# Optimization experiments

Measured on AMD Instinct MI355X. Metric: run time of the kernel, lower is better.

The kernel has to match this reference:

```python
import jax, jax.numpy as jnp
import numpy as np

K = 7            # kernel size per spatial dim
HALF = K // 2    # 3
WIN = K * K      # 49


def _rel_dist():
    # matches torch: meshgrid('ij') of arange(k)-k//2, euclidean dist, flattened row-major
    c = np.arange(K, dtype=np.float32) - HALF
    gi, gj = np.meshgrid(c, c, indexing='ij')
    return jnp.asarray(np.sqrt(gi ** 2 + gj ** 2).reshape(-1))


def _unfold2d(t):
    B, H, W, C = t.shape
    p = jnp.pad(t, ((0, 0), (HALF, HALF), (HALF, HALF), (0, 0)))
    wins = [p[:, i:i + H, j:j + W, :] for i in range(K) for j in range(K)]
    return jnp.stack(wins, axis=3)


def setup_inputs() -> dict:
    key = jax.random.key(0)
    k1, k2, k3, k4, k5 = jax.random.split(key, 5)
    B, H, W, C = 4, 64, 64, 128
    x = jax.random.normal(k1, (B, H, W, C), dtype=jnp.float32)
    W_qkv = jax.random.normal(k2, (C, 3 * C), dtype=jnp.float32) * (C ** -0.5)
    # width_proj is zero-initialized in the module; use small random values to exercise the soft mask
    W_width = jax.random.normal(k3, (C, 1), dtype=jnp.float32) * 0.02
    b_width = jax.random.normal(k4, (1,), dtype=jnp.float32) * 0.02
    W_out = jax.random.normal(k5, (C, C), dtype=jnp.float32) * (C ** -0.5)
    return {"x": x, "W_qkv": W_qkv, "W_width": W_width, "b_width": b_width, "W_out": W_out}


def reference(x, W_qkv, W_width, b_width, W_out):
    B, H, W, C = x.shape
    L = H * W
    scale = C ** -0.5
    rel_dist = _rel_dist()
    max_dist = rel_dist.max()

    qkv = x @ W_qkv                              # (B,H,W,3C)
    q, k, v = jnp.split(qkv, 3, axis=-1)
    width = jax.nn.sigmoid(x @ W_width + b_width) * max_dist + 0.5  # (B,H,W,1)

    k_win = _unfold2d(k).reshape(B, L, WIN, C)
    v_win = _unfold2d(v).reshape(B, L, WIN, C)
    q_flat = q.reshape(B, L, C)
    width_flat = width.reshape(B, L, 1)

    scores = jnp.einsum('blc,blwc->blw', q_flat, k_win) * scale
    soft_mask = jax.nn.sigmoid((width_flat - rel_dist) * 5.0)
    scores = scores - (1.0 - soft_mask) * 10000.0
    attn = jax.nn.softmax(scores, axis=-1)
    out = jnp.einsum('blw,blwc->blc', attn, v_win).reshape(B, H, W, C)
    return (out + v) @ W_out
```

## Files before the change

kernel.cpp:

```cpp
#include <hip/hip_runtime.h>

#define C 128
#define NPIX 16384
#define THREE_C 384

typedef unsigned short u16;
typedef unsigned int u32;
typedef short bf16x8 __attribute__((ext_vector_type(8)));
typedef float f32x4 __attribute__((ext_vector_type(4)));

__device__ __forceinline__ float bf2f(u16 h) { return __uint_as_float(((u32)h) << 16); }
__device__ __forceinline__ u16 f2bf(float f) {
    u32 b = __float_as_uint(f);
    b += 0x7FFF + ((b >> 16) & 1);
    return (u16)(b >> 16);
}
__device__ __forceinline__ u32 pack2(float a, float b) {
    return (u32)f2bf(a) | ((u32)f2bf(b) << 16);
}

#define GST 136

__global__ __launch_bounds__(512) void qkv_kernel(const float* __restrict__ x,
                                                  const float* __restrict__ Wqkv,
                                                  const float* __restrict__ Wwidth,
                                                  const float* __restrict__ bwidth,
                                                  u16* __restrict__ qb,
                                                  u16* __restrict__ kb,
                                                  u16* __restrict__ vb,
                                                  float* __restrict__ width_g) {
    __shared__ u16 xs[128 * GST];
    __shared__ u16 wt[128 * GST];
    const int task = ((int)(blockIdx.x & 7)) * 48 + ((int)blockIdx.x >> 3);
    const int rb = task / 3;
    const int nb = task % 3;
    const int p0 = rb * 128;
    const int tid = threadIdx.x;
    const int wv = tid >> 6;
    const int l = tid & 63;
    const int l15 = l & 15;
    const int l4 = l >> 4;

    for (int f = tid; f < 4096; f += 512) {
        const int kq = f & 31, r = f >> 5;
        const float4 xv = *(const float4*)(x + (size_t)(p0 + r) * C + kq * 4);
        uint2 pk;
        pk.x = pack2(xv.x, xv.y);
        pk.y = pack2(xv.z, xv.w);
        *(uint2*)&xs[r * GST + kq * 4] = pk;
    }
    for (int f = tid; f < 4096; f += 512) {
        const int c = f & 127, kq = f >> 7;
        const float w0 = Wqkv[(size_t)(kq * 4 + 0) * THREE_C + nb * 128 + c];
        const float w1 = Wqkv[(size_t)(kq * 4 + 1) * THREE_C + nb * 128 + c];
        const float w2 = Wqkv[(size_t)(kq * 4 + 2) * THREE_C + nb * 128 + c];
        const float w3 = Wqkv[(size_t)(kq * 4 + 3) * THREE_C + nb * 128 + c];
        uint2 pk;
        pk.x = pack2(w0, w1);
        pk.y = pack2(w2, w3);
        *(uint2*)&wt[c * GST + kq * 4] = pk;
    }
    __syncthreads();

    if (nb == 0 && tid < 128) {
        float wacc = 0.f;
#pragma unroll
        for (int kk = 0; kk < C; ++kk) wacc += bf2f(xs[tid * GST + kk]) * Wwidth[kk];
        const float z = wacc + bwidth[0];
        width_g[p0 + tid] = (1.f / (1.f + __expf(-z))) * 4.242640687f + 0.5f;
    }

    const int strip = wv * 16;
    bf16x8 af[4];
#pragma unroll
    for (int kf = 0; kf < 4; ++kf)
        af[kf] = *(const bf16x8*)&xs[(strip + l15) * GST + kf * 32 + l4 * 8];

    f32x4 acc[8];
#pragma unroll
    for (int nf = 0; nf < 8; ++nf) acc[nf] = (f32x4){0.f, 0.f, 0.f, 0.f};
#pragma unroll
    for (int nf = 0; nf < 8; ++nf) {
#pragma unroll
        for (int kf = 0; kf < 4; ++kf) {
            const bf16x8 bf = *(const bf16x8*)&wt[(nf * 16 + l15) * GST + kf * 32 + l4 * 8];
            acc[nf] = __builtin_amdgcn_mfma_f32_16x16x32_bf16(af[kf], bf, acc[nf], 0, 0, 0);
        }
    }

    u16* dst = (nb == 0) ? qb : (nb == 1) ? kb : vb;
#pragma unroll
    for (int nf = 0; nf < 8; ++nf) {
        const int col = nf * 16 + l15;
#pragma unroll
        for (int r = 0; r < 4; ++r) {
            const int row = strip + l4 * 4 + r;
            dst[(size_t)(p0 + row) * C + col] = f2bf(acc[nf][r]);
        }
    }
}

#define HSTRIDE 136
#define TSTRIDE 232
#define VSWZ(ch, h) ((h) ^ ((((ch) >> 3) & 3) << 3))

__global__ __launch_bounds__(1024) void attn_kernel(const u16* __restrict__ qb,
                                                    const u16* __restrict__ kb,
                                                    const u16* __restrict__ vb,
                                                    const float* __restrict__ width_g,
                                                    const float* __restrict__ Wout,
                                                    float* __restrict__ out) {
    __shared__ u16 Kl[208 * HSTRIDE];
    __shared__ u16 Vt[128 * TSTRIDE];
    __shared__ u16 Pl[64 * TSTRIDE];
    __shared__ float rmax[4][64];
    __shared__ float rsum[4][64];
    __shared__ float wdl[64];

    const int tid = threadIdx.x;
    const int wv = tid >> 6;
    const int l = tid & 63;
    const int l15 = l & 15;
    const int l4 = l >> 4;

    const int W = ((int)blockIdx.x & 7) * 32 + ((int)blockIdx.x >> 3);
    const int b = W >> 6;
    const int t = W & 63;
    const int i0 = (t >> 3) * 8;
    const int j0 = (t & 7) * 8;
    const int pbase = b * 4096;

    if (tid < 64)
        wdl[tid] = width_g[pbase + (i0 + (tid >> 3)) * 64 + j0 + (tid & 7)];

    for (int f = tid; f < 3328; f += 1024) {
        const int c = f & 15, h = f >> 4;
        uint4 val = make_uint4(0, 0, 0, 0);
        if (h < 196) {
            const int hi = (h * 2341) >> 15;
            const int hj = h - hi * 14;
            const int ii = i0 - 3 + hi, jj = j0 - 3 + hj;
            if (((unsigned)ii < 64u) && ((unsigned)jj < 64u))
                val = *(const uint4*)(kb + (size_t)(pbase + ii * 64 + jj) * C + c * 8);
        }
        *(uint4*)&Kl[h * HSTRIDE + c * 8] = val;
    }
    for (int f = tid; f < 1792; f += 1024) {
        const int c8 = f & 15, h2 = f >> 4;
        const int h = h2 * 2;
        union { uint4 u4; u16 us[8]; } va, vz;
        va.u4 = make_uint4(0, 0, 0, 0);
        vz.u4 = make_uint4(0, 0, 0, 0);
        if (h < 196) {
            const int hi = (h * 2341) >> 15;
            const int hj = h - hi * 14;
            const int ii = i0 - 3 + hi, jj = j0 - 3 + hj;
            if (((unsigned)ii < 64u) && ((unsigned)jj < 64u))
                va.u4 = *(const uint4*)(vb + (size_t)(pbase + ii * 64 + jj) * C + c8 * 8);
        }
        if (h + 1 < 196) {
            const int hi = ((h + 1) * 2341) >> 15;
            const int hj = h + 1 - hi * 14;
            const int ii = i0 - 3 + hi, jj = j0 - 3 + hj;
            if (((unsigned)ii < 64u) && ((unsigned)jj < 64u))
                vz.u4 = *(const uint4*)(vb + (size_t)(pbase + ii * 64 + jj) * C + c8 * 8);
        }
#pragma unroll
        for (int s = 0; s < 8; ++s) {
            const int ch = c8 * 8 + s;
            *(u32*)&Vt[ch * TSTRIDE + VSWZ(ch, h)] = (u32)va.us[s] | ((u32)vz.us[s] << 16);
        }
    }

    const int strip = wv >> 2;
    const int g = wv & 3;
    bf16x8 qf[4];
    {
        const int qr = strip * 16 + l15;
        const int p = pbase + (i0 + (qr >> 3)) * 64 + j0 + (qr & 7);
#pragma unroll
        for (int kf = 0; kf < 4; ++kf)
            qf[kf] = *(const bf16x8*)(qb + (size_t)p * C + kf * 32 + l4 * 8);
    }
    __syncthreads();

    f32x4 sv[4];
#pragma unroll
    for (int tt = 0; tt < 4; ++tt) {
        const int nf = g + 4 * tt;
        f32x4 acc = {0.f, 0.f, 0.f, 0.f};
        if (nf < 13) {
            const u16* kr = Kl + (nf * 16 + l15) * HSTRIDE + l4 * 8;
#pragma unroll
            for (int kf = 0; kf < 4; ++kf)
                acc = __builtin_amdgcn_mfma_f32_16x16x32_bf16(
                    qf[kf], *(const bf16x8*)(kr + kf * 32), acc, 0, 0, 0);
        }
        sv[tt] = acc;
    }

    const int qrb = strip * 16 + l4 * 4;
    float wdr[4], mxr[4];
#pragma unroll
    for (int r = 0; r < 4; ++r) { wdr[r] = wdl[qrb + r]; mxr[r] = -3.0e38f; }
#pragma unroll
    for (int tt = 0; tt < 4; ++tt) {
        const int nf = g + 4 * tt;
        if (nf < 13) {
            const int n = nf * 16 + l15;
            const int hi = (n * 2341) >> 15;
            const int hj = n - hi * 14;
#pragma unroll
            for (int r = 0; r < 4; ++r) {
                const int qr = qrb + r;
                const int di = hi - 3 - (qr >> 3);
                const int dj = hj - 3 - (qr & 7);
                const bool valid = ((unsigned)(di + 3) <= 6u) && ((unsigned)(dj + 3) <= 6u);
                float s = -3.0e38f;
                if (valid) {
                    const float rd = sqrtf((float)(di * di + dj * dj));
                    const float sm = 1.f / (1.f + __expf(-5.f * (wdr[r] - rd)));
                    s = sv[tt][r] * 0.08838834765f - (1.f - sm) * 10000.f;
                }
                sv[tt][r] = s;
                mxr[r] = fmaxf(mxr[r], s);
            }
        } else {
#pragma unroll
            for (int r = 0; r < 4; ++r) sv[tt][r] = -3.0e38f;
        }
    }
#pragma unroll
    for (int r = 0; r < 4; ++r) {
        float m = mxr[r];
        m = fmaxf(m, __shfl_xor(m, 1));
        m = fmaxf(m, __shfl_xor(m, 2));
        m = fmaxf(m, __shfl_xor(m, 4));
        m = fmaxf(m, __shfl_xor(m, 8));
        mxr[r] = m;
    }
    float smr[4] = {0.f, 0.f, 0.f, 0.f};
#pragma unroll
    for (int tt = 0; tt < 4; ++tt) {
#pragma unroll
        for (int r = 0; r < 4; ++r) {
            const float e = __expf(sv[tt][r] - mxr[r]);
            sv[tt][r] = e;
            smr[r] += e;
        }
    }
#pragma unroll
    for (int r = 0; r < 4; ++r) {
        float s = smr[r];
        s += __shfl_xor(s, 1);
        s += __shfl_xor(s, 2);
        s += __shfl_xor(s, 4);
        s += __shfl_xor(s, 8);
        smr[r] = s;
    }
    if (l15 == 0) {
#pragma unroll
        for (int r = 0; r < 4; ++r) {
            rmax[g][qrb + r] = mxr[r];
            rsum[g][qrb + r] = smr[r];
        }
    }
    __syncthreads();

    u16* wtl = Kl;
    for (int f = tid; f < 4096; f += 1024) {
        const int c = f & 127, kq = f >> 7;
        const float w0 = Wout[(size_t)(kq * 4 + 0) * C + c];
        const float w1 = Wout[(size_t)(kq * 4 + 1) * C + c];
        const float w2 = Wout[(size_t)(kq * 4 + 2) * C + c];
        const float w3 = Wout[(size_t)(kq * 4 + 3) * C + c];
        uint2 pk;
        pk.x = pack2(w0, w1);
        pk.y = pack2(w2, w3);
        *(uint2*)&wtl[c * GST + kq * 4] = pk;
    }

    float fac[4];
#pragma unroll
    for (int r = 0; r < 4; ++r) {
        const int qr = qrb + r;
        const float m0 = rmax[0][qr], m1 = rmax[1][qr], m2 = rmax[2][qr], m3 = rmax[3][qr];
        const float mf = fmaxf(fmaxf(m0, m1), fmaxf(m2, m3));
        const float tot = rsum[0][qr] * __expf(m0 - mf) + rsum[1][qr] * __expf(m1 - mf)
                        + rsum[2][qr] * __expf(m2 - mf) + rsum[3][qr] * __expf(m3 - mf);
        fac[r] = __expf(mxr[r] - mf) / tot;
    }
#pragma unroll
    for (int tt = 0; tt < 4; ++tt) {
        const int nf = g + 4 * tt;
        if (nf < 13) {
            const int n = nf * 16 + l15;
#pragma unroll
            for (int r = 0; r < 4; ++r)
                Pl[(qrb + r) * TSTRIDE + n] = f2bf(sv[tt][r] * fac[r]);
        } else if (nf == 13) {
            const int n = 208 + l15;
#pragma unroll
            for (int r = 0; r < 4; ++r)
                Pl[(qrb + r) * TSTRIDE + n] = 0;
        }
    }
    __syncthreads();

    f32x4 oacc[2];
    oacc[0] = (f32x4){0.f, 0.f, 0.f, 0.f};
    oacc[1] = (f32x4){0.f, 0.f, 0.f, 0.f};
#pragma unroll
    for (int kf = 0; kf < 7; ++kf) {
        const bf16x8 pa = *(const bf16x8*)(Pl + (strip * 16 + l15) * TSTRIDE + kf * 32 + l4 * 8);
#pragma unroll
        for (int nf2 = 0; nf2 < 2; ++nf2) {
            const int ch = g * 32 + nf2 * 16 + l15;
            const bf16x8 vf = *(const bf16x8*)(Vt + ch * TSTRIDE + VSWZ(ch, kf * 32 + l4 * 8));
            oacc[nf2] = __builtin_amdgcn_mfma_f32_16x16x32_bf16(pa, vf, oacc[nf2], 0, 0, 0);
        }
    }

    u16* ylds = Kl + 128 * GST;
#pragma unroll
    for (int nf2 = 0; nf2 < 2; ++nf2) {
        const int cch = g * 32 + nf2 * 16 + l15;
#pragma unroll
        for (int r = 0; r < 4; ++r) {
            const int qr = qrb + r;
            const int h = 45 + (qr >> 3) * 14 + (qr & 7);
            const float vv = bf2f(Vt[cch * TSTRIDE + VSWZ(cch, h)]);
            ylds[qr * GST + cch] = f2bf(oacc[nf2][r] + vv);
        }
    }
    __syncthreads();

    bf16x8 yf[4];
#pragma unroll
    for (int kf = 0; kf < 4; ++kf)
        yf[kf] = *(const bf16x8*)&ylds[(strip * 16 + l15) * GST + kf * 32 + l4 * 8];

    f32x4 oc[2];
    oc[0] = (f32x4){0.f, 0.f, 0.f, 0.f};
    oc[1] = (f32x4){0.f, 0.f, 0.f, 0.f};
#pragma unroll
    for (int u = 0; u < 2; ++u) {
        const int nf = g + 4 * u;
#pragma unroll
        for (int kf = 0; kf < 4; ++kf) {
            const bf16x8 bf = *(const bf16x8*)&wtl[(nf * 16 + l15) * GST + kf * 32 + l4 * 8];
            oc[u] = __builtin_amdgcn_mfma_f32_16x16x32_bf16(yf[kf], bf, oc[u], 0, 0, 0);
        }
    }
#pragma unroll
    for (int u = 0; u < 2; ++u) {
        const int col = (g + 4 * u) * 16 + l15;
#pragma unroll
        for (int r = 0; r < 4; ++r) {
            const int qr = qrb + r;
            const int p = pbase + (i0 + (qr >> 3)) * 64 + j0 + (qr & 7);
            out[(size_t)p * C + col] = oc[u][r];
        }
    }
}

extern "C" void kernel_launch(void* const* d_in, const int* in_sizes, int n_in,
                              void* d_out, int out_size, void* d_ws, size_t ws_size,
                              hipStream_t stream) {
    const float* x      = (const float*)d_in[0];
    const float* Wqkv   = (const float*)d_in[1];
    const float* Wwidth = (const float*)d_in[2];
    const float* bwidth = (const float*)d_in[3];
    const float* Wout   = (const float*)d_in[4];
    float* out = (float*)d_out;

    u16* qb = (u16*)d_ws;
    u16* kb = qb + (size_t)NPIX * C;
    u16* vb = kb + (size_t)NPIX * C;
    float* width = (float*)(vb + (size_t)NPIX * C);

    qkv_kernel<<<384, 512, 0, stream>>>(x, Wqkv, Wwidth, bwidth, qb, kb, vb, width);
    attn_kernel<<<256, 1024, 0, stream>>>(qb, kb, vb, width, Wout, out);
}
```

Baseline: 29.72 us.

## Split QKV projection into smaller blocks and merge K/V halo gather loops

The QKV projection kernel now processes 64-pixel row tiles with 256 threads, launching 768 blocks instead of 384. This improves occupancy and load balance across compute units, at the cost of reloading each weight slice twice as often. In the attention kernel, the separate K and V halo-gather loops are fused into one fully unrolled loop, so more global loads can be in flight at once. The Wout staging loop is also explicitly unrolled.

```diff
diff --git a/kernel.cpp b/kernel.cpp
--- a/kernel.cpp
+++ b/kernel.cpp
@@ -21,7 +21,7 @@
 
 #define GST 136
 
-__global__ __launch_bounds__(512) void qkv_kernel(const float* __restrict__ x,
+__global__ __launch_bounds__(256) void qkv_kernel(const float* __restrict__ x,
                                                   const float* __restrict__ Wqkv,
                                                   const float* __restrict__ Wwidth,
                                                   const float* __restrict__ bwidth,
@@ -29,19 +29,21 @@
                                                   u16* __restrict__ kb,
                                                   u16* __restrict__ vb,
                                                   float* __restrict__ width_g) {
-    __shared__ u16 xs[128 * GST];
+    __shared__ u16 xs[64 * GST];
     __shared__ u16 wt[128 * GST];
-    const int task = ((int)(blockIdx.x & 7)) * 48 + ((int)blockIdx.x >> 3);
+    const int task = ((int)(blockIdx.x & 7)) * 96 + ((int)blockIdx.x >> 3);
     const int rb = task / 3;
     const int nb = task % 3;
-    const int p0 = rb * 128;
+    const int p0 = rb * 64;
     const int tid = threadIdx.x;
     const int wv = tid >> 6;
     const int l = tid & 63;
     const int l15 = l & 15;
     const int l4 = l >> 4;
 
-    for (int f = tid; f < 4096; f += 512) {
+#pragma unroll
+    for (int t = 0; t < 8; ++t) {
+        const int f = tid + t * 256;
         const int kq = f & 31, r = f >> 5;
         const float4 xv = *(const float4*)(x + (size_t)(p0 + r) * C + kq * 4);
         uint2 pk;
@@ -49,7 +51,9 @@
         pk.y = pack2(xv.z, xv.w);
         *(uint2*)&xs[r * GST + kq * 4] = pk;
     }
-    for (int f = tid; f < 4096; f += 512) {
+#pragma unroll
+    for (int t = 0; t < 16; ++t) {
+        const int f = tid + t * 256;
         const int c = f & 127, kq = f >> 7;
         const float w0 = Wqkv[(size_t)(kq * 4 + 0) * THREE_C + nb * 128 + c];
         const float w1 = Wqkv[(size_t)(kq * 4 + 1) * THREE_C + nb * 128 + c];
@@ -62,7 +66,7 @@
     }
     __syncthreads();
 
-    if (nb == 0 && tid < 128) {
+    if (nb == 0 && tid < 64) {
         float wacc = 0.f;
 #pragma unroll
         for (int kk = 0; kk < C; ++kk) wacc += bf2f(xs[tid * GST + kk]) * Wwidth[kk];
@@ -133,42 +137,46 @@
     if (tid < 64)
         wdl[tid] = width_g[pbase + (i0 + (tid >> 3)) * 64 + j0 + (tid & 7)];
 
-    for (int f = tid; f < 3328; f += 1024) {
-        const int c = f & 15, h = f >> 4;
-        uint4 val = make_uint4(0, 0, 0, 0);
-        if (h < 196) {
-            const int hi = (h * 2341) >> 15;
-            const int hj = h - hi * 14;
-            const int ii = i0 - 3 + hi, jj = j0 - 3 + hj;
-            if (((unsigned)ii < 64u) && ((unsigned)jj < 64u))
-                val = *(const uint4*)(kb + (size_t)(pbase + ii * 64 + jj) * C + c * 8);
-        }
-        *(uint4*)&Kl[h * HSTRIDE + c * 8] = val;
-    }
-    for (int f = tid; f < 1792; f += 1024) {
-        const int c8 = f & 15, h2 = f >> 4;
-        const int h = h2 * 2;
-        union { uint4 u4; u16 us[8]; } va, vz;
-        va.u4 = make_uint4(0, 0, 0, 0);
-        vz.u4 = make_uint4(0, 0, 0, 0);
-        if (h < 196) {
-            const int hi = (h * 2341) >> 15;
-            const int hj = h - hi * 14;
-            const int ii = i0 - 3 + hi, jj = j0 - 3 + hj;
-            if (((unsigned)ii < 64u) && ((unsigned)jj < 64u))
-                va.u4 = *(const uint4*)(vb + (size_t)(pbase + ii * 64 + jj) * C + c8 * 8);
-        }
-        if (h + 1 < 196) {
-            const int hi = ((h + 1) * 2341) >> 15;
-            const int hj = h + 1 - hi * 14;
-            const int ii = i0 - 3 + hi, jj = j0 - 3 + hj;
-            if (((unsigned)ii < 64u) && ((unsigned)jj < 64u))
-                vz.u4 = *(const uint4*)(vb + (size_t)(pbase + ii * 64 + jj) * C + c8 * 8);
-        }
-#pragma unroll
-        for (int s = 0; s < 8; ++s) {
-            const int ch = c8 * 8 + s;
-            *(u32*)&Vt[ch * TSTRIDE + VSWZ(ch, h)] = (u32)va.us[s] | ((u32)vz.us[s] << 16);
+#pragma unroll
+    for (int u = 0; u < 5; ++u) {
+        const int f = tid + u * 1024;
+        if (f < 3328) {
+            const int c = f & 15, h = f >> 4;
+            uint4 val = make_uint4(0, 0, 0, 0);
+            if (h < 196) {
+                const int hi = (h * 2341) >> 15;
+                const int hj = h - hi * 14;
+                const int ii = i0 - 3 + hi, jj = j0 - 3 + hj;
+                if (((unsigned)ii < 64u) && ((unsigned)jj < 64u))
+                    val = *(const uint4*)(kb + (size_t)(pbase + ii * 64 + jj) * C + c * 8);
+            }
+            *(uint4*)&Kl[h * HSTRIDE + c * 8] = val;
+        } else {
+            const int f2 = f - 3328;
+            const int c8 = f2 & 15, h = (f2 >> 4) * 2;
+            union { uint4 u4; u16 us[8]; } va, vz;
+            va.u4 = make_uint4(0, 0, 0, 0);
+            vz.u4 = make_uint4(0, 0, 0, 0);
+            {
+                const int hi = (h * 2341) >> 15;
+                const int hj = h - hi * 14;
+                const int ii = i0 - 3 + hi, jj = j0 - 3 + hj;
+                if ((h < 196) && ((unsigned)ii < 64u) && ((unsigned)jj < 64u))
+                    va.u4 = *(const uint4*)(vb + (size_t)(pbase + ii * 64 + jj) * C + c8 * 8);
+            }
+            {
+                const int h1 = h + 1;
+                const int hi = (h1 * 2341) >> 15;
+                const int hj = h1 - hi * 14;
+                const int ii = i0 - 3 + hi, jj = j0 - 3 + hj;
+                if ((h1 < 196) && ((unsigned)ii < 64u) && ((unsigned)jj < 64u))
+                    vz.u4 = *(const uint4*)(vb + (size_t)(pbase + ii * 64 + jj) * C + c8 * 8);
+            }
+#pragma unroll
+            for (int s = 0; s < 8; ++s) {
+                const int ch = c8 * 8 + s;
+                *(u32*)&Vt[ch * TSTRIDE + VSWZ(ch, h)] = (u32)va.us[s] | ((u32)vz.us[s] << 16);
+            }
         }
     }
 
@@ -268,7 +276,9 @@
     __syncthreads();
 
     u16* wtl = Kl;
-    for (int f = tid; f < 4096; f += 1024) {
+#pragma unroll
+    for (int tq = 0; tq < 4; ++tq) {
+        const int f = tid + tq * 1024;
         const int c = f & 127, kq = f >> 7;
         const float w0 = Wout[(size_t)(kq * 4 + 0) * C + c];
         const float w1 = Wout[(size_t)(kq * 4 + 1) * C + c];
@@ -379,6 +389,6 @@
     u16* vb = kb + (size_t)NPIX * C;
     float* width = (float*)(vb + (size_t)NPIX * C);
 
-    qkv_kernel<<<384, 512, 0, stream>>>(x, Wqkv, Wwidth, bwidth, qb, kb, vb, width);
+    qkv_kernel<<<768, 256, 0, stream>>>(x, Wqkv, Wwidth, bwidth, qb, kb, vb, width);
     attn_kernel<<<256, 1024, 0, stream>>>(qb, kb, vb, width, Wout, out);
 }
```

Measured after the change: 30.01 us. No clear change (+1.0%).
